# Kernel tuning notes

Hardware: AMD Instinct MI355X
Metric: run time of the kernel (lower is better)

## Reference

```python
import jax, jax.numpy as jnp
import numpy as np
from jax import lax

EPS = 1e-12
N_ITER = 25
PAD = 1
GROUPS = 4


def conv2d(x, w, padding, groups):
    # x: NCHW, w: OIHW (I = C // groups)
    return lax.conv_general_dilated(
        x, w, (1, 1), ((padding, padding), (padding, padding)),
        dimension_numbers=('NCHW', 'OIHW', 'NCHW'), feature_group_count=groups)


def conv_transpose2d(h, w, padding, groups):
    # stride-1 transposed conv == conv with spatially flipped, in/out-swapped kernel
    O, Ig, kh, kw = w.shape
    I = Ig * groups
    wt = w.reshape(groups, O // groups, Ig, kh, kw).transpose(0, 2, 1, 3, 4)
    wt = wt.reshape(I, O // groups, kh, kw)[:, :, ::-1, ::-1]
    return conv2d(h, wt, kh - 1 - padding, groups)


def nnmf_conv2d(x, weight, n_iterations=N_ITER, padding=PAD, groups=GROUPS,
                normalize_channels=True):
    # non-negative, L1-normalized (per output channel) weights
    w = jnp.abs(weight)
    w = w / (w.sum(axis=(1, 2, 3), keepdims=True) + EPS)
    # non-negative input, normalized over channels
    x = x / (x.sum(axis=1, keepdims=True) + EPS)
    N, C, H, W = x.shape
    O = weight.shape[0]
    h0 = jnp.full((N, O, H, W), 1.0 / O, dtype=x.dtype)

    def body(i, h):
        recon = conv_transpose2d(h, w, padding, groups)   # back-projection
        ratio = x / (recon + EPS)
        h = h * conv2d(ratio, w, padding, groups)         # multiplicative update
        if normalize_channels:
            h = h / (h.sum(axis=1, keepdims=True) + EPS)
        return h

    return lax.fori_loop(0, n_iterations, body, h0)


def layernorm_cf(x, w, b, eps=1e-6):
    # channels_first LayerNorm over C of NCHW
    u = x.mean(axis=1, keepdims=True)
    s = jnp.mean((x - u) ** 2, axis=1, keepdims=True)
    xn = (x - u) * lax.rsqrt(s + eps)
    return w[None, :, None, None] * xn + b[None, :, None, None]


def layernorm_last(x, w, b, eps=1e-5):
    u = x.mean(axis=-1, keepdims=True)
    s = jnp.mean((x - u) ** 2, axis=-1, keepdims=True)
    return (x - u) * lax.rsqrt(s + eps) * w + b


def setup_inputs() -> dict:
    key = jax.random.key(0)
    ks = jax.random.split(key, 8)
    C, Hd = 96, 384  # dim, mlp hidden = 4*embed_dim
    x = jax.random.normal(ks[0], (8, C, 56, 56), dtype=jnp.float32)
    return {
        'x': x,
        'ln1_w': jnp.ones((C,), jnp.float32),
        'ln1_b': jnp.zeros((C,), jnp.float32),
        'w_nnmf': jax.random.uniform(ks[1], (C, C // GROUPS, 3, 3), jnp.float32, 0.01, 1.0),
        'ln2_w': jnp.ones((C,), jnp.float32),
        'ln2_b': jnp.zeros((C,), jnp.float32),
        'w1': jax.random.normal(ks[2], (C, Hd), jnp.float32) * 0.02,
        'b1': jnp.zeros((Hd,), jnp.float32),
        'w2': jax.random.normal(ks[3], (Hd, C), jnp.float32) * 0.02,
        'b2': jnp.zeros((C,), jnp.float32),
    }


def reference(x, ln1_w, ln1_b, w_nnmf, ln2_w, ln2_b, w1, b1, w2, b2):
    # attn branch (NNMF conv on relu'd channels-first layernorm)
    x_norm = layernorm_cf(x, ln1_w, ln1_b)
    x = x + nnmf_conv2d(jax.nn.relu(x_norm), w_nnmf)
    # MLP branch, channels-last
    xl = jnp.transpose(x, (0, 2, 3, 1))  # NHWC
    h = layernorm_last(xl, ln2_w, ln2_b)
    h = jax.nn.gelu(h @ w1 + b1, approximate=False) @ w2 + b2
    xl = xl + h
    return jnp.transpose(xl, (0, 3, 1, 2))
```

## Files before the change

kernel.cpp:

```cpp
#include <hip/hip_runtime.h>
#include <math.h>
#include <string.h>

typedef unsigned short ushort_t;
typedef __attribute__((ext_vector_type(8))) short bhalf8;
typedef __attribute__((ext_vector_type(4))) float floatx4;

#define NN    8
#define CC_   96
#define HH    56
#define WW    56
#define HWHW  (HH*WW)
#define NPIX  (NN*HWHW)
#define NELEM (NN*CC_*HWHW)
#define GROUPS 4
#define IG    24
#define NITER 25
#define EPSV  1e-12f
#define TS    40

__device__ __forceinline__ unsigned bf2pack(float a, float b) {
    unsigned ua = __float_as_uint(a), ub = __float_as_uint(b);
    ua += 0x7fffu + ((ua >> 16) & 1u);
    ub += 0x7fffu + ((ub >> 16) & 1u);
    return (ua >> 16) | (ub & 0xffff0000u);
}
__device__ __forceinline__ ushort_t bf1pack(float a) {
    unsigned ua = __float_as_uint(a);
    ua += 0x7fffu + ((ua >> 16) & 1u);
    return (ushort_t)(ua >> 16);
}
__device__ __forceinline__ float bflo(unsigned u) { return __uint_as_float(u << 16); }
__device__ __forceinline__ float bfhi(unsigned u) { return __uint_as_float(u & 0xffff0000u); }

__device__ __forceinline__ float rcpf(float x) {
    float r;
    asm("v_rcp_f32 %0, %1" : "=v"(r) : "v"(x));
    return r;
}

__device__ __forceinline__ int swz(int slot, int u) {
    return slot*TS + ((((u >> 3) ^ (slot >> 3)) & 3) << 3) + (u & 7);
}

__global__ void wnorm_n_kernel(const float* __restrict__ w_in, float* __restrict__ Wn) {
    int o = blockIdx.x;
    int t = threadIdx.x;
    float myv = (t < 216) ? fabsf(w_in[o*216 + t]) : 0.f;
    float v = myv;
    #pragma unroll
    for (int off = 32; off; off >>= 1) v += __shfl_down(v, off, 64);
    __shared__ float red[4];
    if ((t & 63) == 0) red[t >> 6] = v;
    __syncthreads();
    float s = red[0] + red[1] + red[2] + red[3];
    if (t < 216) Wn[o*216 + t] = myv / (s + EPSV);
}

__global__ void wpack_kernel(const float* __restrict__ Wn,
                             ushort_t* __restrict__ WfP, ushort_t* __restrict__ WtP) {
    int bi = blockIdx.x;
    int sel = bi / 72;
    int rem = bi % 72;
    int ot = rem & 1;
    int gt = rem >> 1;
    int g = gt / 9, tap = gt % 9;
    int lane = threadIdx.x;
    int quad = lane >> 4, nn = lane & 15;
    int m = ot*16 + nn;
    ushort_t v[8];
    #pragma unroll
    for (int j = 0; j < 8; ++j) {
        int kc = quad*8 + j;
        float val = 0.f;
        if (m < IG && kc < IG) {
            if (sel == 0) val = Wn[(g*IG + m)*216 + kc*9 + tap];
            else          val = Wn[(g*IG + kc)*216 + m*9 + (8 - tap)];
        }
        v[j] = bf1pack(val);
    }
    ushort_t* dst = (sel ? WtP : WfP) + ((size_t)(gt*2 + ot)*64 + lane)*8;
    *(uint4*)dst = *(uint4*)v;
}

__global__ void mlppack_kernel(const float* __restrict__ w1, const float* __restrict__ w2,
                               ushort_t* __restrict__ w1P, ushort_t* __restrict__ w2P) {
    int f = blockIdx.x;
    int lane = threadIdx.x;
    int quad = lane >> 4, nn = lane & 15;
    ushort_t v[8];
    if (f < 72) {
        int nt = f / 3, ks = f % 3;
        #pragma unroll
        for (int j = 0; j < 8; ++j)
            v[j] = bf1pack(w1[(size_t)(ks*32 + quad*8 + j)*384 + nt*16 + nn]);
        *(uint4*)(w1P + ((size_t)f*64 + lane)*8) = *(uint4*)v;
    } else {
        int f2 = f - 72;
        int mt = f2 / 12, ks = f2 % 12;
        #pragma unroll
        for (int j = 0; j < 8; ++j)
            v[j] = bf1pack(w2[(size_t)(ks*32 + quad*8 + j)*96 + mt*16 + nn]);
        *(uint4*)(w2P + ((size_t)f2*64 + lane)*8) = *(uint4*)v;
    }
}

__global__ void ln1_kernel(const float* __restrict__ x, const float* __restrict__ lw,
                           const float* __restrict__ lb, unsigned* __restrict__ Xp) {
    int p = blockIdx.x * blockDim.x + threadIdx.x;
    if (p >= NPIX) return;
    int n = p / HWHW, hw = p % HWHW;
    const float* xp = x + (size_t)n*CC_*HWHW + hw;
    float s = 0.f, ss = 0.f;
    for (int c = 0; c < CC_; ++c) { float v = xp[(size_t)c*HWHW]; s += v; ss += v*v; }
    float u  = s * (1.f/CC_);
    float var = ss * (1.f/CC_) - u*u;
    float rs = rsqrtf(var + 1e-6f);
    float sr = 0.f;
    for (int c = 0; c < CC_; ++c) {
        float v = xp[(size_t)c*HWHW];
        float a = fmaxf((v-u)*rs*lw[c] + lb[c], 0.f);
        sr += a;
    }
    float inv = 1.f / (sr + EPSV);
    for (int c = 0; c < CC_; c += 2) {
        float v0 = xp[(size_t)c*HWHW];
        float v1 = xp[(size_t)(c+1)*HWHW];
        float a0 = fmaxf((v0-u)*rs*lw[c] + lb[c], 0.f) * inv;
        float a1 = fmaxf((v1-u)*rs*lw[c+1] + lb[c+1], 0.f) * inv;
        int g = c / IG, pr = (c % IG) >> 1;
        Xp[(size_t)((n*4+g)*12 + pr)*HWHW + hw] = bf2pack(a0, a1);
    }
}

__global__ __launch_bounds__(512, 4) void nnmf_mfma_kernel(
        const unsigned* __restrict__ HupI, unsigned* __restrict__ HupO,
        const float* __restrict__ Scur, float* __restrict__ Snxt,
        const ushort_t* __restrict__ WtP, const ushort_t* __restrict__ WfP,
        const unsigned* __restrict__ Xp,
        int it0, unsigned huInit, float sInit) {
    __shared__ ushort_t hn[352*TS];
    __shared__ ushort_t rt_[288*TS];
    __shared__ float sinv[352];
    __shared__ float sacc[392];
    int b    = blockIdx.x;
    int k_   = b >> 3;
    int ng   = (b & 7)*4 + (k_ >> 4);
    int tile = k_ & 15;
    int rtb  = tile >> 1;
    int half = tile & 1;
    int n    = ng >> 2;
    int g    = ng & 3;
    int tid  = threadIdx.x;
    int r0   = rtb*7;
    int xb   = half*28;
    unsigned planeBase = (unsigned)(n*4 + g)*12;

    int waveId = tid >> 6, lane = tid & 63;
    int quad = lane >> 4, nn = lane & 15;
    int otB = waveId & 1;
    int mbB = otB*16 + quad*4;

    bhalf8 afrB[9];
    {
        const ushort_t* ap = WtP + ((size_t)(g*9*2 + otB)*64 + lane)*8;
        #pragma unroll
        for (int t = 0; t < 9; ++t) afrB[t] = *(const bhalf8*)(ap + (size_t)t*2*64*8);
    }

    uint2 raw[5];
    #pragma unroll
    for (int kk = 0; kk < 5; ++kk) {
        int idx  = tid + kk*512;
        int pr2  = idx / 352;
        int slot = idx - pr2*352;
        int r = slot >> 5, q = slot & 31;
        int gr = r0 - 2 + r, gc = xb - 2 + q;
        uint2 rv = {0u, 0u};
        if (!it0 && pr2 < 6 && gr >= 0 && gr < HH && gc >= 0 && gc < WW) {
            unsigned off = (unsigned)(gr*WW + gc);
            rv.x = HupI[(size_t)(planeBase + 2*pr2)*HWHW + off];
            rv.y = HupI[(size_t)(planeBase + 2*pr2 + 1)*HWHW + off];
        }
        raw[kk] = rv;
    }

    if (tid < 352) {
        int r = tid >> 5, q = tid & 31;
        int gr = r0 - 2 + r, gc = xb - 2 + q;
        float st = 1.f;
        if (gr >= 0 && gr < HH && gc >= 0 && gc < WW) {
            if (it0) {
                st = 4.f*sInit;
            } else {
                unsigned p = (unsigned)(n*HWHW + gr*WW + gc);
                st = Scur[p] + Scur[NPIX+p] + Scur[2*NPIX+p] + Scur[3*NPIX+p];
            }
        }
        sinv[tid] = rcpf(st + EPSV);
    }
    __syncthreads();

    #pragma unroll
    for (int kk = 0; kk < 6; ++kk) {
        int idx  = tid + kk*512;
        if (idx < 2816) {
            int pr2  = idx / 352;
            int slot = idx - pr2*352;
            int r = slot >> 5, q = slot & 31;
            int gr = r0 - 2 + r, gc = xb - 2 + q;
            uint2 pk = {0u, 0u};
            if (pr2 < 6 && gr >= 0 && gr < HH && gc >= 0 && gc < WW) {
                float si = sinv[slot];
                if (it0) {
                    float hval = bflo(huInit) * si;
                    pk.x = bf2pack(hval, hval);
                    pk.y = pk.x;
                } else {
                    pk.x = bf2pack(bflo(raw[kk].x)*si, bfhi(raw[kk].x)*si);
                    pk.y = bf2pack(bflo(raw[kk].y)*si, bfhi(raw[kk].y)*si);
                }
            }
            *(uint2*)&hn[swz(slot, 4*pr2)] = pk;
        }
    }
    if (tid < 288) *(uint4*)&rt_[swz(tid, 24)] = (uint4){0u,0u,0u,0u};
    __syncthreads();

    {
        #pragma unroll
        for (int i = 0; i < 5; ++i) {
            int tk = waveId + 8*i;
            if (tk < 36) {
                int pt  = (tk >> 1) & 1;
                int row = tk >> 2;
                int x0R = pt*14;
                unsigned xa = 0u, xc = 0u;
                int gr = r0 - 1 + row, gc = xb - 1 + x0R + nn;
                if (mbB < IG && gr >= 0 && gr < HH && gc >= 0 && gc < WW) {
                    unsigned off = (unsigned)(gr*WW + gc);
                    unsigned pb = planeBase + (unsigned)(mbB >> 1);
                    xa = Xp[(size_t)pb*HWHW + off];
                    xc = Xp[(size_t)(pb+1)*HWHW + off];
                }
                floatx4 acc = (floatx4){0.f,0.f,0.f,0.f};
                #pragma unroll
                for (int t = 0; t < 9; ++t) {
                    int ky = t / 3, kx = t % 3;
                    bhalf8 bfr = *(const bhalf8*)
                        &hn[swz((row + ky)*32 + kx + nn + x0R, quad*8)];
                    acc = __builtin_amdgcn_mfma_f32_16x16x32_bf16(afrB[t], bfr, acc, 0, 0, 0);
                }
                if (mbB < IG) {
                    int slot = row*32 + x0R + nn;
                    *(unsigned*)&rt_[swz(slot, mbB)] =
                        bf2pack(bflo(xa)*rcpf(acc[0]+EPSV), bfhi(xa)*rcpf(acc[1]+EPSV));
                    *(unsigned*)&rt_[swz(slot, mbB + 2)] =
                        bf2pack(bflo(xc)*rcpf(acc[2]+EPSV), bfhi(xc)*rcpf(acc[3]+EPSV));
                }
            }
        }
    }
    __syncthreads();

    {
        const ushort_t* ap = WfP + ((size_t)(g*9*2 + otB)*64 + lane)*8;
        bhalf8 afr[9];
        #pragma unroll
        for (int t = 0; t < 9; ++t) afr[t] = *(const bhalf8*)(ap + (size_t)t*2*64*8);
        int mb = mbB;

        #pragma unroll
        for (int i = 0; i < 4; ++i) {
            int tc = waveId + 8*i;
            if (tc < 28) {
                int xt = (tc >> 1) & 1;
                int w  = tc >> 2;
                int px0 = xt*12;
                floatx4 acc = (floatx4){0.f,0.f,0.f,0.f};
                #pragma unroll
                for (int t = 0; t < 9; ++t) {
                    int ky = t / 3, kx = t % 3;
                    bhalf8 bfr = *(const bhalf8*)
                        &rt_[swz((w + ky)*32 + kx + nn + px0, quad*8)];
                    acc = __builtin_amdgcn_mfma_f32_16x16x32_bf16(afr[t], bfr, acc, 0, 0, 0);
                }

                int grow = r0 + w;
                int pxh = px0 + nn;
                float psum = 0.f;
                if (mb < IG) {
                    unsigned off = (unsigned)(grow*WW + xb + pxh);
                    unsigned pb = planeBase + (unsigned)(mb >> 1);
                    uint2 hv = *(const uint2*)&hn[swz((w + 2)*32 + pxh + 2, mb)];
                    float h0 = bflo(hv.x) * acc[0];
                    float h1 = bfhi(hv.x) * acc[1];
                    float h2 = bflo(hv.y) * acc[2];
                    float h3 = bfhi(hv.y) * acc[3];
                    HupO[(size_t)pb*HWHW + off]     = bf2pack(h0, h1);
                    HupO[(size_t)(pb+1)*HWHW + off] = bf2pack(h2, h3);
                    psum = h0 + h1 + h2 + h3;
                }
                psum += __shfl_down(psum, 32, 64);
                psum += __shfl_down(psum, 16, 64);
                if (lane < 16) sacc[otB*196 + w*28 + pxh] = psum;
            }
        }
    }
    __syncthreads();
    if (tid < 196) {
        Snxt[(size_t)g*NPIX + n*HWHW + (r0 + tid/28)*WW + xb + (tid % 28)]
            = sacc[tid] + sacc[196 + tid];
    }
}

__global__ void resln4_kernel(const float* __restrict__ x, const unsigned* __restrict__ Hup,
                              const float* __restrict__ S4,
                              const float* __restrict__ lw, const float* __restrict__ lb,
                              float* __restrict__ out, unsigned* __restrict__ XLNt) {
    int p = blockIdx.x * blockDim.x + threadIdx.x;
    if (p >= NPIX) return;
    int n = p / HWHW, hw = p % HWHW;
    size_t base = (size_t)n*CC_*HWHW + hw;
    float stot = S4[p] + S4[NPIX+p] + S4[2*NPIX+p] + S4[3*NPIX+p];
    float sinv = 1.f / (stot + EPSV);
    float s = 0.f, ss = 0.f;
    for (int c = 0; c < CC_; c += 2) {
        int g = c / IG, pr = (c % IG) >> 1;
        unsigned hu = Hup[(size_t)((n*4+g)*12 + pr)*HWHW + hw];
        float v0 = x[base + (size_t)c*HWHW]     + bflo(hu) * sinv;
        float v1 = x[base + (size_t)(c+1)*HWHW] + bfhi(hu) * sinv;
        out[base + (size_t)c*HWHW]     = v0;
        out[base + (size_t)(c+1)*HWHW] = v1;
        s += v0 + v1; ss += v0*v0 + v1*v1;
    }
    float u  = s * (1.f/CC_);
    float var = ss * (1.f/CC_) - u*u;
    float rs = rsqrtf(var + 1e-5f);
    for (int c = 0; c < CC_; c += 2) {
        float v0 = out[base + (size_t)c*HWHW];
        float v1 = out[base + (size_t)(c+1)*HWHW];
        float a0 = (v0-u)*rs*lw[c]   + lb[c];
        float a1 = (v1-u)*rs*lw[c+1] + lb[c+1];
        XLNt[(size_t)p*48 + (c >> 1)] = bf2pack(a0, a1);
    }
}

__global__ __launch_bounds__(128) void mlp5_kernel(
        const ushort_t* __restrict__ XLNt, const ushort_t* __restrict__ w1P,
        const float* __restrict__ b1, const ushort_t* __restrict__ w2P,
        const float* __restrict__ b2, float* __restrict__ out) {
    __shared__ ushort_t lh[16*392];
    int blk = blockIdx.x;
    int tid = threadIdx.x;
    int wv  = tid >> 6, lane = tid & 63;
    int quad = lane >> 4, nn = lane & 15;
    int p0  = blk * 16;
    int n   = p0 / HWHW;
    int hw0 = p0 % HWHW;

    const ushort_t* xrow = XLNt + (size_t)(p0 + nn)*96 + quad*8;
    bhalf8 a1[3];
    #pragma unroll
    for (int ks = 0; ks < 3; ++ks) a1[ks] = *(const bhalf8*)(xrow + ks*32);

    #pragma unroll 1
    for (int i = 0; i < 12; ++i) {
        int nt = wv*12 + i;
        floatx4 acc = (floatx4){0.f,0.f,0.f,0.f};
        #pragma unroll
        for (int ks = 0; ks < 3; ++ks) {
            bhalf8 bfr = *(const bhalf8*)(w1P + ((size_t)(nt*3 + ks)*64 + lane)*8);
            acc = __builtin_amdgcn_mfma_f32_16x16x32_bf16(a1[ks], bfr, acc, 0, 0, 0);
        }
        float b1v = b1[nt*16 + nn];
        #pragma unroll
        for (int r = 0; r < 4; ++r) {
            float h = acc[r] + b1v;
            h = 0.5f * h * (1.f + erff(h * 0.70710678118654752440f));
            lh[(quad*4 + r)*392 + nt*16 + nn] = bf1pack(h);
        }
    }
    __syncthreads();

    bhalf8 bf2[12];
    #pragma unroll
    for (int ks = 0; ks < 12; ++ks)
        bf2[ks] = *(const bhalf8*)&lh[nn*392 + ks*32 + quad*8];

    #pragma unroll 1
    for (int i = 0; i < 3; ++i) {
        int mt = wv*3 + i;
        floatx4 acc = (floatx4){0.f,0.f,0.f,0.f};
        #pragma unroll
        for (int ks = 0; ks < 12; ++ks) {
            bhalf8 af = *(const bhalf8*)(w2P + ((size_t)(mt*12 + ks)*64 + lane)*8);
            acc = __builtin_amdgcn_mfma_f32_16x16x32_bf16(af, bf2[ks], acc, 0, 0, 0);
        }
        #pragma unroll
        for (int r = 0; r < 4; ++r) {
            int c = mt*16 + quad*4 + r;
            size_t addr = ((size_t)n*CC_ + c)*HWHW + hw0 + nn;
            out[addr] += acc[r] + b2[c];
        }
    }
}

extern "C" void kernel_launch(void* const* d_in, const int* in_sizes, int n_in,
                              void* d_out, int out_size, void* d_ws, size_t ws_size,
                              hipStream_t stream) {
    const float* x    = (const float*)d_in[0];
    const float* ln1w = (const float*)d_in[1];
    const float* ln1b = (const float*)d_in[2];
    const float* wnn  = (const float*)d_in[3];
    const float* ln2w = (const float*)d_in[4];
    const float* ln2b = (const float*)d_in[5];
    const float* w1   = (const float*)d_in[6];
    const float* b1   = (const float*)d_in[7];
    const float* w2   = (const float*)d_in[8];
    const float* b2   = (const float*)d_in[9];
    float* out = (float*)d_out;
    char* ws = (char*)d_ws;

    float*    Wn   = (float*)ws;                      ws += 20736*4;
    ushort_t* WfP  = (ushort_t*)ws;                   ws += 73728*2;
    ushort_t* WtP  = (ushort_t*)ws;                   ws += 73728*2;
    ushort_t* w1P  = (ushort_t*)ws;                   ws += 36864*2;
    ushort_t* w2P  = (ushort_t*)ws;                   ws += 36864*2;
    unsigned* Xp   = (unsigned*)ws;                   ws += (size_t)(NELEM/2)*4;
    unsigned* Hu0  = (unsigned*)ws;                   ws += (size_t)(NELEM/2)*4;
    unsigned* Hu1  = (unsigned*)ws;                   ws += (size_t)(NELEM/2)*4;
    float*    SA   = (float*)ws;                      ws += (size_t)4*NPIX*4;
    float*    SB   = (float*)ws;                      ws += (size_t)4*NPIX*4;
    unsigned* XLNt = (unsigned*)ws;                   ws += (size_t)NPIX*48*4;

    union { float f; unsigned u; } cv; cv.f = 1.f/96.f;
    unsigned ur = cv.u + 0x7fffu + ((cv.u >> 16) & 1u);
    unsigned short hbits = (unsigned short)(ur >> 16);
    unsigned huInit = ((unsigned)hbits << 16) | hbits;
    union { float f; unsigned u; } hv; hv.u = ((unsigned)hbits) << 16;
    float sInit = 24.f * hv.f;

    wnorm_n_kernel<<<CC_, 256, 0, stream>>>(wnn, Wn);
    wpack_kernel<<<144, 64, 0, stream>>>(Wn, WfP, WtP);
    mlppack_kernel<<<144, 64, 0, stream>>>(w1, w2, w1P, w2P);
    ln1_kernel<<<NPIX/256, 256, 0, stream>>>(x, ln1w, ln1b, Xp);

    for (int it = 0; it < NITER; ++it) {
        const unsigned* HuI  = (it & 1) ? Hu1 : Hu0;
        unsigned*       HuO  = (it & 1) ? Hu0 : Hu1;
        const float*    Scur = (it & 1) ? SB : SA;
        float*          Snxt = (it & 1) ? SA : SB;
        nnmf_mfma_kernel<<<512, 512, 0, stream>>>(HuI, HuO, Scur, Snxt, WtP, WfP, Xp,
                                                  (it == 0) ? 1 : 0, huInit, sInit);
    }

    resln4_kernel<<<NPIX/256, 256, 0, stream>>>(x, Hu1, SB, ln2w, ln2b, out, XLNt);
    mlp5_kernel<<<NPIX/16, 128, 0, stream>>>((const ushort_t*)XLNt, w1P, b1, w2P, b2, out);
}
```

Before: 434.3 us.

## Fuse prep kernels into one, fuse residual LayerNorm into MLP, drop sinv staging

Folds weight normalization, NNMF weight packing, MLP weight packing and LN1 into a single prep launch. Fuses the residual-add plus LayerNorm2 step into the MLP kernel through shared memory, so the XLNt workspace round trip and the read-modify-write of the output both go away. In the NNMF iteration kernel, the shared sinv array and its barrier are removed: each thread now loads the four channel-sum partials itself and computes the reciprocal in registers. That trades one block-wide sync for redundant global loads of the sums across the six plane pairs.

```diff
diff --git a/kernel.cpp b/kernel.cpp
--- a/kernel.cpp
+++ b/kernel.cpp
@@ -43,93 +43,100 @@
     return slot*TS + ((((u >> 3) ^ (slot >> 3)) & 3) << 3) + (u & 7);
 }
 
-__global__ void wnorm_n_kernel(const float* __restrict__ w_in, float* __restrict__ Wn) {
-    int o = blockIdx.x;
-    int t = threadIdx.x;
-    float myv = (t < 216) ? fabsf(w_in[o*216 + t]) : 0.f;
-    float v = myv;
-    #pragma unroll
-    for (int off = 32; off; off >>= 1) v += __shfl_down(v, off, 64);
-    __shared__ float red[4];
-    if ((t & 63) == 0) red[t >> 6] = v;
-    __syncthreads();
-    float s = red[0] + red[1] + red[2] + red[3];
-    if (t < 216) Wn[o*216 + t] = myv / (s + EPSV);
-}
-
-__global__ void wpack_kernel(const float* __restrict__ Wn,
-                             ushort_t* __restrict__ WfP, ushort_t* __restrict__ WtP) {
-    int bi = blockIdx.x;
-    int sel = bi / 72;
-    int rem = bi % 72;
-    int ot = rem & 1;
-    int gt = rem >> 1;
-    int g = gt / 9, tap = gt % 9;
-    int lane = threadIdx.x;
-    int quad = lane >> 4, nn = lane & 15;
-    int m = ot*16 + nn;
-    ushort_t v[8];
-    #pragma unroll
-    for (int j = 0; j < 8; ++j) {
-        int kc = quad*8 + j;
-        float val = 0.f;
-        if (m < IG && kc < IG) {
-            if (sel == 0) val = Wn[(g*IG + m)*216 + kc*9 + tap];
-            else          val = Wn[(g*IG + kc)*216 + m*9 + (8 - tap)];
-        }
-        v[j] = bf1pack(val);
-    }
-    ushort_t* dst = (sel ? WtP : WfP) + ((size_t)(gt*2 + ot)*64 + lane)*8;
-    *(uint4*)dst = *(uint4*)v;
-}
-
-__global__ void mlppack_kernel(const float* __restrict__ w1, const float* __restrict__ w2,
-                               ushort_t* __restrict__ w1P, ushort_t* __restrict__ w2P) {
-    int f = blockIdx.x;
-    int lane = threadIdx.x;
-    int quad = lane >> 4, nn = lane & 15;
-    ushort_t v[8];
-    if (f < 72) {
-        int nt = f / 3, ks = f % 3;
-        #pragma unroll
-        for (int j = 0; j < 8; ++j)
-            v[j] = bf1pack(w1[(size_t)(ks*32 + quad*8 + j)*384 + nt*16 + nn]);
-        *(uint4*)(w1P + ((size_t)f*64 + lane)*8) = *(uint4*)v;
+__global__ __launch_bounds__(256) void prep_kernel(
+        const float* __restrict__ w_in,
+        ushort_t* __restrict__ WfP, ushort_t* __restrict__ WtP,
+        const float* __restrict__ w1, const float* __restrict__ w2,
+        ushort_t* __restrict__ w1P, ushort_t* __restrict__ w2P,
+        const float* __restrict__ x, const float* __restrict__ lw1,
+        const float* __restrict__ lb1, unsigned* __restrict__ Xp) {
+    __shared__ float wn[24*216];
+    __shared__ float rsum[24];
+    int b = blockIdx.x;
+    int tid = threadIdx.x;
+
+    if (b < 4) {
+        int g = b;
+        if (tid < 24) {
+            const float* wr = w_in + (size_t)(g*24 + tid)*216;
+            float s = 0.f;
+            for (int j = 0; j < 216; ++j) s += fabsf(wr[j]);
+            rsum[tid] = s;
+        }
+        __syncthreads();
+        for (int i = tid; i < 24*216; i += 256) {
+            int row = i / 216;
+            wn[i] = fabsf(w_in[(size_t)g*24*216 + i]) * rcpf(rsum[row] + EPSV);
+        }
+        __syncthreads();
+        int lg = tid >> 6;
+        int lane = tid & 63;
+        int quad = lane >> 4, nn15 = lane & 15;
+        #pragma unroll 1
+        for (int i = 0; i < 9; ++i) {
+            int fr  = lg + 4*i;
+            int sel = fr / 18;
+            int rem = fr % 18;
+            int ot  = rem & 1;
+            int tap = rem >> 1;
+            int m = ot*16 + nn15;
+            ushort_t v[8];
+            #pragma unroll
+            for (int j = 0; j < 8; ++j) {
+                int kc = quad*8 + j;
+                float val = 0.f;
+                if (m < IG && kc < IG) {
+                    if (sel == 0) val = wn[m*216 + kc*9 + tap];
+                    else          val = wn[kc*216 + m*9 + (8 - tap)];
+                }
+                v[j] = bf1pack(val);
+            }
+            ushort_t* dst = (sel ? WtP : WfP) + ((size_t)((g*9 + tap)*2 + ot)*64 + lane)*8;
+            *(uint4*)dst = *(uint4*)v;
+        }
+    } else if (b < 40) {
+        int f = (b - 4)*4 + (tid >> 6);
+        int lane = tid & 63;
+        int quad = lane >> 4, nn15 = lane & 15;
+        ushort_t v[8];
+        if (f < 72) {
+            int nt = f / 3, ks = f % 3;
+            #pragma unroll
+            for (int j = 0; j < 8; ++j)
+                v[j] = bf1pack(w1[(size_t)(ks*32 + quad*8 + j)*384 + nt*16 + nn15]);
+            *(uint4*)(w1P + ((size_t)f*64 + lane)*8) = *(uint4*)v;
+        } else {
+            int f2 = f - 72;
+            int mt = f2 / 12, ks = f2 % 12;
+            #pragma unroll
+            for (int j = 0; j < 8; ++j)
+                v[j] = bf1pack(w2[(size_t)(ks*32 + quad*8 + j)*96 + mt*16 + nn15]);
+            *(uint4*)(w2P + ((size_t)f2*64 + lane)*8) = *(uint4*)v;
+        }
     } else {
-        int f2 = f - 72;
-        int mt = f2 / 12, ks = f2 % 12;
-        #pragma unroll
-        for (int j = 0; j < 8; ++j)
-            v[j] = bf1pack(w2[(size_t)(ks*32 + quad*8 + j)*96 + mt*16 + nn]);
-        *(uint4*)(w2P + ((size_t)f2*64 + lane)*8) = *(uint4*)v;
-    }
-}
-
-__global__ void ln1_kernel(const float* __restrict__ x, const float* __restrict__ lw,
-                           const float* __restrict__ lb, unsigned* __restrict__ Xp) {
-    int p = blockIdx.x * blockDim.x + threadIdx.x;
-    if (p >= NPIX) return;
-    int n = p / HWHW, hw = p % HWHW;
-    const float* xp = x + (size_t)n*CC_*HWHW + hw;
-    float s = 0.f, ss = 0.f;
-    for (int c = 0; c < CC_; ++c) { float v = xp[(size_t)c*HWHW]; s += v; ss += v*v; }
-    float u  = s * (1.f/CC_);
-    float var = ss * (1.f/CC_) - u*u;
-    float rs = rsqrtf(var + 1e-6f);
-    float sr = 0.f;
-    for (int c = 0; c < CC_; ++c) {
-        float v = xp[(size_t)c*HWHW];
-        float a = fmaxf((v-u)*rs*lw[c] + lb[c], 0.f);
-        sr += a;
-    }
-    float inv = 1.f / (sr + EPSV);
-    for (int c = 0; c < CC_; c += 2) {
-        float v0 = xp[(size_t)c*HWHW];
-        float v1 = xp[(size_t)(c+1)*HWHW];
-        float a0 = fmaxf((v0-u)*rs*lw[c] + lb[c], 0.f) * inv;
-        float a1 = fmaxf((v1-u)*rs*lw[c+1] + lb[c+1], 0.f) * inv;
-        int g = c / IG, pr = (c % IG) >> 1;
-        Xp[(size_t)((n*4+g)*12 + pr)*HWHW + hw] = bf2pack(a0, a1);
+        int p = (b - 40)*256 + tid;
+        int n = p / HWHW, hw = p % HWHW;
+        const float* xp = x + (size_t)n*CC_*HWHW + hw;
+        float s = 0.f, ss = 0.f;
+        for (int c = 0; c < CC_; ++c) { float v = xp[(size_t)c*HWHW]; s += v; ss += v*v; }
+        float u  = s * (1.f/CC_);
+        float var = ss * (1.f/CC_) - u*u;
+        float rs = rsqrtf(var + 1e-6f);
+        float sr = 0.f;
+        for (int c = 0; c < CC_; ++c) {
+            float v = xp[(size_t)c*HWHW];
+            float a = fmaxf((v-u)*rs*lw1[c] + lb1[c], 0.f);
+            sr += a;
+        }
+        float inv = 1.f / (sr + EPSV);
+        for (int c = 0; c < CC_; c += 2) {
+            float v0 = xp[(size_t)c*HWHW];
+            float v1 = xp[(size_t)(c+1)*HWHW];
+            float a0 = fmaxf((v0-u)*rs*lw1[c] + lb1[c], 0.f) * inv;
+            float a1 = fmaxf((v1-u)*rs*lw1[c+1] + lb1[c+1], 0.f) * inv;
+            int g = c / IG, pr = (c % IG) >> 1;
+            Xp[(size_t)((n*4+g)*12 + pr)*HWHW + hw] = bf2pack(a0, a1);
+        }
     }
 }
 
@@ -141,7 +148,6 @@
         int it0, unsigned huInit, float sInit) {
     __shared__ ushort_t hn[352*TS];
     __shared__ ushort_t rt_[288*TS];
-    __shared__ float sinv[352];
     __shared__ float sacc[392];
     int b    = blockIdx.x;
     int k_   = b >> 3;
@@ -168,42 +174,36 @@
         for (int t = 0; t < 9; ++t) afrB[t] = *(const bhalf8*)(ap + (size_t)t*2*64*8);
     }
 
-    uint2 raw[5];
-    #pragma unroll
-    for (int kk = 0; kk < 5; ++kk) {
-        int idx  = tid + kk*512;
-        int pr2  = idx / 352;
-        int slot = idx - pr2*352;
-        int r = slot >> 5, q = slot & 31;
-        int gr = r0 - 2 + r, gc = xb - 2 + q;
-        uint2 rv = {0u, 0u};
-        if (!it0 && pr2 < 6 && gr >= 0 && gr < HH && gc >= 0 && gc < WW) {
-            unsigned off = (unsigned)(gr*WW + gc);
-            rv.x = HupI[(size_t)(planeBase + 2*pr2)*HWHW + off];
-            rv.y = HupI[(size_t)(planeBase + 2*pr2 + 1)*HWHW + off];
-        }
-        raw[kk] = rv;
-    }
-
-    if (tid < 352) {
-        int r = tid >> 5, q = tid & 31;
-        int gr = r0 - 2 + r, gc = xb - 2 + q;
-        float st = 1.f;
-        if (gr >= 0 && gr < HH && gc >= 0 && gc < WW) {
-            if (it0) {
-                st = 4.f*sInit;
-            } else {
-                unsigned p = (unsigned)(n*HWHW + gr*WW + gc);
-                st = Scur[p] + Scur[NPIX+p] + Scur[2*NPIX+p] + Scur[3*NPIX+p];
-            }
-        }
-        sinv[tid] = rcpf(st + EPSV);
-    }
-    __syncthreads();
-
+    uint2 raw[6];
+    float sA[6], sB[6], sC[6], sD[6];
     #pragma unroll
     for (int kk = 0; kk < 6; ++kk) {
-        int idx  = tid + kk*512;
+        int idx = tid + kk*512;
+        uint2 rv = {0u, 0u};
+        float a0 = 0.f, a1 = 0.f, a2 = 0.f, a3 = 0.f;
+        if (idx < 2816) {
+            int pr2  = idx / 352;
+            int slot = idx - pr2*352;
+            int r = slot >> 5, q = slot & 31;
+            int gr = r0 - 2 + r, gc = xb - 2 + q;
+            if (!it0 && pr2 < 6 && gr >= 0 && gr < HH && gc >= 0 && gc < WW) {
+                unsigned off = (unsigned)(gr*WW + gc);
+                unsigned pix = (unsigned)(n*HWHW) + off;
+                rv.x = HupI[(size_t)(planeBase + 2*pr2)*HWHW + off];
+                rv.y = HupI[(size_t)(planeBase + 2*pr2 + 1)*HWHW + off];
+                a0 = Scur[pix];
+                a1 = Scur[NPIX + pix];
+                a2 = Scur[2*NPIX + pix];
+                a3 = Scur[3*NPIX + pix];
+            }
+        }
+        raw[kk] = rv;
+        sA[kk] = a0; sB[kk] = a1; sC[kk] = a2; sD[kk] = a3;
+    }
+
+    #pragma unroll
+    for (int kk = 0; kk < 6; ++kk) {
+        int idx = tid + kk*512;
         if (idx < 2816) {
             int pr2  = idx / 352;
             int slot = idx - pr2*352;
@@ -211,12 +211,14 @@
             int gr = r0 - 2 + r, gc = xb - 2 + q;
             uint2 pk = {0u, 0u};
             if (pr2 < 6 && gr >= 0 && gr < HH && gc >= 0 && gc < WW) {
-                float si = sinv[slot];
                 if (it0) {
+                    float si = rcpf(4.f*sInit + EPSV);
                     float hval = bflo(huInit) * si;
                     pk.x = bf2pack(hval, hval);
                     pk.y = pk.x;
                 } else {
+                    float st = sA[kk] + sB[kk] + sC[kk] + sD[kk];
+                    float si = rcpf(st + EPSV);
                     pk.x = bf2pack(bflo(raw[kk].x)*si, bfhi(raw[kk].x)*si);
                     pk.y = bf2pack(bflo(raw[kk].y)*si, bfhi(raw[kk].y)*si);
                 }
@@ -314,55 +316,74 @@
     }
 }
 
-__global__ void resln4_kernel(const float* __restrict__ x, const unsigned* __restrict__ Hup,
-                              const float* __restrict__ S4,
-                              const float* __restrict__ lw, const float* __restrict__ lb,
-                              float* __restrict__ out, unsigned* __restrict__ XLNt) {
-    int p = blockIdx.x * blockDim.x + threadIdx.x;
-    if (p >= NPIX) return;
-    int n = p / HWHW, hw = p % HWHW;
-    size_t base = (size_t)n*CC_*HWHW + hw;
-    float stot = S4[p] + S4[NPIX+p] + S4[2*NPIX+p] + S4[3*NPIX+p];
-    float sinv = 1.f / (stot + EPSV);
-    float s = 0.f, ss = 0.f;
-    for (int c = 0; c < CC_; c += 2) {
-        int g = c / IG, pr = (c % IG) >> 1;
-        unsigned hu = Hup[(size_t)((n*4+g)*12 + pr)*HWHW + hw];
-        float v0 = x[base + (size_t)c*HWHW]     + bflo(hu) * sinv;
-        float v1 = x[base + (size_t)(c+1)*HWHW] + bfhi(hu) * sinv;
-        out[base + (size_t)c*HWHW]     = v0;
-        out[base + (size_t)(c+1)*HWHW] = v1;
-        s += v0 + v1; ss += v0*v0 + v1*v1;
-    }
-    float u  = s * (1.f/CC_);
-    float var = ss * (1.f/CC_) - u*u;
-    float rs = rsqrtf(var + 1e-5f);
-    for (int c = 0; c < CC_; c += 2) {
-        float v0 = out[base + (size_t)c*HWHW];
-        float v1 = out[base + (size_t)(c+1)*HWHW];
-        float a0 = (v0-u)*rs*lw[c]   + lb[c];
-        float a1 = (v1-u)*rs*lw[c+1] + lb[c+1];
-        XLNt[(size_t)p*48 + (c >> 1)] = bf2pack(a0, a1);
-    }
-}
-
-__global__ __launch_bounds__(128) void mlp5_kernel(
-        const ushort_t* __restrict__ XLNt, const ushort_t* __restrict__ w1P,
-        const float* __restrict__ b1, const ushort_t* __restrict__ w2P,
-        const float* __restrict__ b2, float* __restrict__ out) {
+__global__ __launch_bounds__(128) void mlpres_kernel(
+        const float* __restrict__ x, const unsigned* __restrict__ Hup,
+        const float* __restrict__ S4,
+        const float* __restrict__ lw, const float* __restrict__ lb,
+        const ushort_t* __restrict__ w1P, const float* __restrict__ b1,
+        const ushort_t* __restrict__ w2P, const float* __restrict__ b2,
+        float* __restrict__ out) {
     __shared__ ushort_t lh[16*392];
+    __shared__ unsigned xln[16*52];
+    __shared__ float vt[96*18];
+    __shared__ float redS[8*16], redSS[8*16];
+    __shared__ float uArr[16], rsArr[16];
     int blk = blockIdx.x;
     int tid = threadIdx.x;
-    int wv  = tid >> 6, lane = tid & 63;
-    int quad = lane >> 4, nn = lane & 15;
     int p0  = blk * 16;
     int n   = p0 / HWHW;
     int hw0 = p0 % HWHW;
 
-    const ushort_t* xrow = XLNt + (size_t)(p0 + nn)*96 + quad*8;
+    {
+        int px = tid & 15, cg = tid >> 4;
+        int p  = p0 + px, hw = hw0 + px;
+        float stot = S4[p] + S4[NPIX+p] + S4[2*NPIX+p] + S4[3*NPIX+p];
+        float sinv = 1.f / (stot + EPSV);
+        int g = cg >> 1;
+        unsigned plane = (unsigned)(n*4 + g)*12 + (unsigned)((cg & 1)*6);
+        size_t xbase = (size_t)n*CC_*HWHW + hw;
+        float v[12];
+        float s = 0.f, ss = 0.f;
+        #pragma unroll
+        for (int j = 0; j < 6; ++j) {
+            int c = cg*12 + 2*j;
+            unsigned hu = Hup[(size_t)(plane + j)*HWHW + hw];
+            float v0 = x[xbase + (size_t)c*HWHW]     + bflo(hu) * sinv;
+            float v1 = x[xbase + (size_t)(c+1)*HWHW] + bfhi(hu) * sinv;
+            v[2*j] = v0; v[2*j+1] = v1;
+            s += v0 + v1; ss += v0*v0 + v1*v1;
+        }
+        redS[cg*16 + px] = s; redSS[cg*16 + px] = ss;
+        __syncthreads();
+        if (tid < 16) {
+            float S_ = 0.f, SS_ = 0.f;
+            #pragma unroll
+            for (int k = 0; k < 8; ++k) { S_ += redS[k*16 + tid]; SS_ += redSS[k*16 + tid]; }
+            float u  = S_ * (1.f/CC_);
+            float var = SS_ * (1.f/CC_) - u*u;
+            uArr[tid] = u; rsArr[tid] = rsqrtf(var + 1e-5f);
+        }
+        __syncthreads();
+        float u = uArr[px], rs = rsArr[px];
+        #pragma unroll
+        for (int j = 0; j < 6; ++j) {
+            int c = cg*12 + 2*j;
+            float a0 = (v[2*j]   - u)*rs*lw[c]   + lb[c];
+            float a1 = (v[2*j+1] - u)*rs*lw[c+1] + lb[c+1];
+            xln[px*52 + cg*6 + j] = bf2pack(a0, a1);
+            vt[c*18 + px]     = v[2*j];
+            vt[(c+1)*18 + px] = v[2*j+1];
+        }
+    }
+    __syncthreads();
+
+    int wv  = tid >> 6, lane = tid & 63;
+    int quad = lane >> 4, nn = lane & 15;
+
     bhalf8 a1[3];
     #pragma unroll
-    for (int ks = 0; ks < 3; ++ks) a1[ks] = *(const bhalf8*)(xrow + ks*32);
+    for (int ks = 0; ks < 3; ++ks)
+        a1[ks] = *(const bhalf8*)&xln[nn*52 + ks*16 + quad*4];
 
     #pragma unroll 1
     for (int i = 0; i < 12; ++i) {
@@ -401,7 +422,7 @@
         for (int r = 0; r < 4; ++r) {
             int c = mt*16 + quad*4 + r;
             size_t addr = ((size_t)n*CC_ + c)*HWHW + hw0 + nn;
-            out[addr] += acc[r] + b2[c];
+            out[addr] = vt[c*18 + nn] + (acc[r] + b2[c]);
         }
     }
 }
@@ -422,7 +443,6 @@
     float* out = (float*)d_out;
     char* ws = (char*)d_ws;
 
-    float*    Wn   = (float*)ws;                      ws += 20736*4;
     ushort_t* WfP  = (ushort_t*)ws;                   ws += 73728*2;
     ushort_t* WtP  = (ushort_t*)ws;                   ws += 73728*2;
     ushort_t* w1P  = (ushort_t*)ws;                   ws += 36864*2;
@@ -432,7 +452,6 @@
     unsigned* Hu1  = (unsigned*)ws;                   ws += (size_t)(NELEM/2)*4;
     float*    SA   = (float*)ws;                      ws += (size_t)4*NPIX*4;
     float*    SB   = (float*)ws;                      ws += (size_t)4*NPIX*4;
-    unsigned* XLNt = (unsigned*)ws;                   ws += (size_t)NPIX*48*4;
 
     union { float f; unsigned u; } cv; cv.f = 1.f/96.f;
     unsigned ur = cv.u + 0x7fffu + ((cv.u >> 16) & 1u);
@@ -441,10 +460,8 @@
     union { float f; unsigned u; } hv; hv.u = ((unsigned)hbits) << 16;
     float sInit = 24.f * hv.f;
 
-    wnorm_n_kernel<<<CC_, 256, 0, stream>>>(wnn, Wn);
-    wpack_kernel<<<144, 64, 0, stream>>>(Wn, WfP, WtP);
-    mlppack_kernel<<<144, 64, 0, stream>>>(w1, w2, w1P, w2P);
-    ln1_kernel<<<NPIX/256, 256, 0, stream>>>(x, ln1w, ln1b, Xp);
+    prep_kernel<<<138, 256, 0, stream>>>(wnn, WfP, WtP, w1, w2, w1P, w2P,
+                                         x, ln1w, ln1b, Xp);
 
     for (int it = 0; it < NITER; ++it) {
         const unsigned* HuI  = (it & 1) ? Hu1 : Hu0;
@@ -455,6 +472,6 @@
                                                   (it == 0) ? 1 : 0, huInit, sInit);
     }
 
-    resln4_kernel<<<NPIX/256, 256, 0, stream>>>(x, Hu1, SB, ln2w, ln2b, out, XLNt);
-    mlp5_kernel<<<NPIX/16, 128, 0, stream>>>((const ushort_t*)XLNt, w1P, b1, w2P, b2, out);
-}
+    mlpres_kernel<<<NPIX/16, 128, 0, stream>>>(x, Hu1, SB, ln2w, ln2b,
+                                               w1P, b1, w2P, b2, out);
+}
```

Measured after the change: 402.7 us. -7.3%, faster.
